# Optimization experiments

Measured on AMD Instinct MI355X. Metric: run time of the kernel, lower is better.

## Reference

```python
import jax, jax.numpy as jnp
import numpy as np
from jax import lax

T, B, C, H, W, NH = 4, 4, 512, 32, 32, 8
HD = C // NH  # head dim 64
EPS = 1e-5
TAU = 2.0

@jax.custom_vjp
def spike(x):
    # Heaviside forward (spikingjelly: x >= 0 -> 1)
    return (x >= 0.0).astype(x.dtype)

def _spike_fwd(x):
    return spike(x), x

def _spike_bwd(x, g):
    # sigmoid surrogate gradient, alpha=4.0 (spikingjelly default)
    s = jax.nn.sigmoid(4.0 * x)
    return (g * 4.0 * s * (1.0 - s),)

spike.defvjp(_spike_fwd, _spike_bwd)

def lif(x, v_th=1.0):
    # MultiStepLIFNode: tau=2, v_reset=0 (hard reset), detach_reset=True.
    # x: [T, ...]; sequential over T via scan.
    def step(v, xt):
        v = v + (xt - v) / TAU
        s = spike(v - v_th)
        v = v * (1.0 - lax.stop_gradient(s))  # detach_reset hard reset
        return v, s
    return lax.scan(step, jnp.zeros_like(x[0]), x)[1]

def bn(x, g, b, m, v):
    # eval-mode BatchNorm1d over channel axis 2 of [T,B,C,N]
    scale = g / jnp.sqrt(v + EPS)
    return (x - m[:, None]) * scale[:, None] + b[:, None]

def setup_inputs() -> dict:
    key = jax.random.key(0)
    ks = jax.random.split(key, 24)
    def w(k):
        return jax.random.normal(k, (C, C), jnp.float32) * (1.0 / np.sqrt(C))
    def bnp(k):
        k1, k2, k3, k4 = jax.random.split(k, 4)
        return (jax.random.normal(k1, (C,), jnp.float32) * 0.1 + 1.0,
                jax.random.normal(k2, (C,), jnp.float32) * 0.1,
                jax.random.normal(k3, (C,), jnp.float32) * 0.1,
                jax.random.uniform(k4, (C,), jnp.float32, 0.5, 1.5))
    q_g, q_b, q_m, q_v = bnp(ks[1])
    k_g, k_b, k_m, k_v = bnp(ks[3])
    v_g, v_b, v_m, v_v = bnp(ks[5])
    p_g, p_b, p_m, p_v = bnp(ks[7])
    return {
        'x': jax.random.normal(ks[0], (T, B, C, H, W), jnp.float32),
        'Wq': w(ks[10]), 'q_g': q_g, 'q_b': q_b, 'q_m': q_m, 'q_v': q_v,
        'Wk': w(ks[11]), 'k_g': k_g, 'k_b': k_b, 'k_m': k_m, 'k_v': k_v,
        'Wv': w(ks[12]), 'v_g': v_g, 'v_b': v_b, 'v_m': v_m, 'v_v': v_v,
        'Wp': w(ks[13]), 'bp': jax.random.normal(ks[14], (C,), jnp.float32) * 0.02,
        'p_g': p_g, 'p_b': p_b, 'p_m': p_m, 'p_v': p_v,
    }

def reference(x, Wq, q_g, q_b, q_m, q_v, Wk, k_g, k_b, k_m, k_v,
              Wv, v_g, v_b, v_m, v_v, Wp, bp, p_g, p_b, p_m, p_v):
    t, b, c, h, w = x.shape
    n = h * w
    xs = lif(x).reshape(t, b, c, n)  # proj_lif -> spikes in {0,1}

    def qkv_branch(Wt, g, bb, m, v):
        y = jnp.einsum('tbcn,dc->tbdn', xs, Wt)  # conv1x1
        y = lif(bn(y, g, bb, m, v))               # bn + lif
        # [T,B,C,N] -> [T,B,heads,N,head_dim]
        return y.reshape(t, b, NH, HD, n).transpose(0, 1, 2, 4, 3)

    q = qkv_branch(Wq, q_g, q_b, q_m, q_v)
    k = qkv_branch(Wk, k_g, k_b, k_m, k_v)
    v = qkv_branch(Wv, v_g, v_b, v_m, v_v)

    attn = jnp.einsum('tbhnd,tbhmd->tbhnm', q, k)           # q @ k^T (binary spikes)
    o = jnp.einsum('tbhnm,tbhmd->tbhnd', attn, v) * 0.125   # attn @ v * 0.125
    o = o.transpose(0, 1, 2, 4, 3).reshape(t, b, c, n)      # [T,B,C,N]
    o = lif(o, v_th=0.5)                                     # attn_lif

    y = jnp.einsum('tbcn,dc->tbdn', o, Wp) + bp[:, None]     # proj conv (bias)
    y = bn(y, p_g, p_b, p_m, p_v)
    return y.reshape(t, b, c, h, w)
```

## Files before the change

kernel.cpp:

```cpp
#include <hip/hip_runtime.h>
#include <hip/hip_bf16.h>
#include <stdint.h>

#define T_  4
#define B_  4
#define C_  512
#define N_  1024
#define NH_ 8
#define HD_ 64
#define NP_ 16384
#define EPS_ 1e-5f

typedef __bf16 bf16_t;
typedef __bf16 bf16x8 __attribute__((ext_vector_type(8)));
typedef float  f32x4  __attribute__((ext_vector_type(4)));
typedef unsigned short u16x4 __attribute__((ext_vector_type(4)));
typedef unsigned char  u8x4  __attribute__((ext_vector_type(4)));
typedef unsigned long long u64;
typedef unsigned int u32;

#define XS_OFF   0ULL
#define AHI_OFF  16777216ULL
#define ALO_OFF  18350080ULL
#define PHI_OFF  19922944ULL
#define PLO_OFF  20447232ULL
#define SC_OFF   20971520ULL
#define SH_OFF   20977664ULL
#define PSC_OFF  20983808ULL
#define PSH_OFF  20985856ULL
#define QS_OFF   20987904ULL
#define KB_OFF   37765120ULL
#define VB_OFF   38813696ULL
#define M2H_OFF  39862272ULL
#define M2L_OFF  40910848ULL

__global__ __launch_bounds__(256) void prep_kernel(
    const float* __restrict__ Wq, const float* __restrict__ Wk,
    const float* __restrict__ Wv, const float* __restrict__ Wp,
    const float* __restrict__ qg, const float* __restrict__ qb, const float* __restrict__ qm, const float* __restrict__ qv,
    const float* __restrict__ kg, const float* __restrict__ kb, const float* __restrict__ km, const float* __restrict__ kv,
    const float* __restrict__ vg, const float* __restrict__ vb, const float* __restrict__ vm, const float* __restrict__ vv,
    const float* __restrict__ bp,
    const float* __restrict__ pg, const float* __restrict__ pb, const float* __restrict__ pm, const float* __restrict__ pv,
    bf16_t* __restrict__ Ahi, bf16_t* __restrict__ Alo,
    bf16_t* __restrict__ Phi, bf16_t* __restrict__ Plo,
    float* __restrict__ scale, float* __restrict__ shift,
    float* __restrict__ pscale, float* __restrict__ pshift)
{
    const int i0 = blockIdx.x * 256 + threadIdx.x;
    const int stride = gridDim.x * 256;
    for (int idx = i0; idx < 1536 * 512; idx += stride) {
        int r = idx >> 9;
        int br = r >> 9;
        const float* W = (br == 0) ? Wq : (br == 1) ? Wk : Wv;
        float w = W[((r & 511) << 9) + (idx & 511)];
        bf16_t h = (bf16_t)w;
        Ahi[idx] = h;
        Alo[idx] = (bf16_t)(w - (float)h);
    }
    for (int idx = i0; idx < 512 * 512; idx += stride) {
        float w = Wp[idx];
        bf16_t h = (bf16_t)w;
        Phi[idx] = h;
        Plo[idx] = (bf16_t)(w - (float)h);
    }
    for (int idx = i0; idx < 1536; idx += stride) {
        int br = idx >> 9, d = idx & 511;
        const float* g  = (br == 0) ? qg : (br == 1) ? kg : vg;
        const float* bb = (br == 0) ? qb : (br == 1) ? kb : vb;
        const float* mm = (br == 0) ? qm : (br == 1) ? km : vm;
        const float* vr = (br == 0) ? qv : (br == 1) ? kv : vv;
        float sc = g[d] / sqrtf(vr[d] + EPS_);
        scale[idx] = sc;
        shift[idx] = bb[d] - mm[d] * sc;
    }
    for (int idx = i0; idx < 512; idx += stride) {
        float sc = pg[idx] / sqrtf(pv[idx] + EPS_);
        pscale[idx] = sc;
        pshift[idx] = (bp[idx] - pm[idx]) * sc + pb[idx];
    }
}

__global__ __launch_bounds__(256) void lif_x_kernel(const float* __restrict__ x,
                                                    bf16_t* __restrict__ xsT)
{
    __shared__ bf16_t St[64 * 72];
    const int tid = threadIdx.x;
    const int nl  = tid & 63;
    const int c4  = tid >> 6;
    const int n0 = blockIdx.x * 64;
    const int c0 = blockIdx.y * 64;
    const int b  = blockIdx.z;
    float v[16];
#pragma unroll
    for (int k = 0; k < 16; ++k) v[k] = 0.f;

    for (int t = 0; t < T_; ++t) {
        bf16x8 s0, s1;
#pragma unroll
        for (int k = 0; k < 16; ++k) {
            float xv = x[(size_t)((t * B_ + b) * C_ + (c0 + c4 * 16 + k)) * N_ + n0 + nl];
            float vn = v[k] + (xv - v[k]) * 0.5f;
            bool s = (vn >= 1.0f);
            v[k] = s ? 0.0f : vn;
            bf16_t sp = s ? (bf16_t)1.0f : (bf16_t)0.0f;
            if (k < 8) s0[k] = sp; else s1[k - 8] = sp;
        }
        __syncthreads();
        *(bf16x8*)&St[nl * 72 + c4 * 16]     = s0;
        *(bf16x8*)&St[nl * 72 + c4 * 16 + 8] = s1;
        __syncthreads();
#pragma unroll
        for (int it = 0; it < 2; ++it) {
            int id = it * 256 + tid;
            int row = id >> 3, sg = id & 7;
            *(bf16x8*)&xsT[((size_t)((t * B_ + b) << 10) + n0 + row) * C_ + c0 + sg * 8] =
                *(const bf16x8*)&St[row * 72 + sg * 8];
        }
    }
}

__global__ __launch_bounds__(256) void gemm_qkv_lif(
    const bf16_t* __restrict__ Ahi, const bf16_t* __restrict__ Alo,
    const bf16_t* __restrict__ xsT,
    const float* __restrict__ scale, const float* __restrict__ shift,
    bf16_t* __restrict__ qsT, u32* __restrict__ kbits, u32* __restrict__ vbits)
{
    __shared__ __align__(16) unsigned char smem[49152];

    const int tid  = threadIdx.x;
    const int lane = tid & 63;
    const int wv   = tid >> 6;
    const int wr   = wv >> 1, wc = wv & 1;
    const int m0   = blockIdx.y * 128;
    const int branch = m0 >> 9;
    const int site0 = blockIdx.x * 32;
    const int b    = site0 >> 10;
    const int n0   = site0 & 1023;

    const int frow = lane & 15;
    const int g4   = lane >> 4;

    f32x4 acc[4][4];
#pragma unroll
    for (int t = 0; t < 4; ++t)
#pragma unroll
        for (int mi = 0; mi < 4; ++mi) acc[t][mi] = f32x4{0.f, 0.f, 0.f, 0.f};

    for (int kk = 0; kk < 512; kk += 64) {
        __syncthreads();
#pragma unroll
        for (int p = 0; p < 4; ++p) {
            int s = p * 256 + tid;
            int row = s >> 3, j = s & 7;
            int kc = (j ^ (row & 7)) << 3;
            size_t goff = (size_t)(m0 + row) * 512 + kk + kc;
            unsigned ldsb = (unsigned)(p * 256 + wv * 64) * 16;
            __builtin_amdgcn_global_load_lds((const __attribute__((address_space(1))) void*)(Ahi + goff),
                                             (__attribute__((address_space(3))) void*)(smem + ldsb), 16, 0, 0);
            __builtin_amdgcn_global_load_lds((const __attribute__((address_space(1))) void*)(Alo + goff),
                                             (__attribute__((address_space(3))) void*)(smem + 16384 + ldsb), 16, 0, 0);
        }
#pragma unroll
        for (int p = 0; p < 4; ++p) {
            int s = p * 256 + tid;
            int t = s >> 8, row = (s >> 3) & 31, j = s & 7;
            int kc = (j ^ (row & 7)) << 3;
            size_t goff = ((size_t)((t * B_ + b) << 10) + n0 + row) * 512 + kk + kc;
            unsigned ldsb = 32768u + (unsigned)(p * 256 + wv * 64) * 16;
            __builtin_amdgcn_global_load_lds((const __attribute__((address_space(1))) void*)(xsT + goff),
                                             (__attribute__((address_space(3))) void*)(smem + ldsb), 16, 0, 0);
        }
        __syncthreads();

#pragma unroll
        for (int ks = 0; ks < 2; ++ks) {
            bf16x8 ah[4], al[4];
#pragma unroll
            for (int mi = 0; mi < 4; ++mi) {
                int row = wr * 64 + mi * 16 + frow;
                int jj = (ks * 4 + g4) ^ (row & 7);
                ah[mi] = *(const bf16x8*)(smem + row * 128 + jj * 16);
                al[mi] = *(const bf16x8*)(smem + 16384 + row * 128 + jj * 16);
            }
#pragma unroll
            for (int t = 0; t < 4; ++t) {
                int rowb = wc * 16 + frow;
                int jj = (ks * 4 + g4) ^ (rowb & 7);
                bf16x8 bb = *(const bf16x8*)(smem + 32768 + t * 4096 + rowb * 128 + jj * 16);
#pragma unroll
                for (int mi = 0; mi < 4; ++mi) {
                    acc[t][mi] = __builtin_amdgcn_mfma_f32_16x16x32_bf16(ah[mi], bb, acc[t][mi], 0, 0, 0);
                    acc[t][mi] = __builtin_amdgcn_mfma_f32_16x16x32_bf16(al[mi], bb, acc[t][mi], 0, 0, 0);
                }
            }
        }
    }

    if (branch == 0) {
        bf16_t* Tt = (bf16_t*)smem;
        u16x4 qpk[4][4];
#pragma unroll
        for (int mi = 0; mi < 4; ++mi)
#pragma unroll
            for (int r = 0; r < 4; ++r) {
                int gr = m0 + wr * 64 + mi * 16 + g4 * 4 + r;
                float sc = scale[gr], sh = shift[gr];
                float vv = 0.f;
#pragma unroll
                for (int t = 0; t < 4; ++t) {
                    float y = acc[t][mi][r] * sc + sh;
                    float vn = vv + (y - vv) * 0.5f;
                    bool s = (vn >= 1.0f);
                    vv = s ? 0.f : vn;
                    qpk[t][mi][r] = s ? 0x3F80 : 0;
                }
            }
#pragma unroll
        for (int t = 0; t < 4; ++t) {
            const int tb = t * B_ + b;
            __syncthreads();
#pragma unroll
            for (int mi = 0; mi < 4; ++mi) {
                int nl = wc * 16 + frow;
                int cl = wr * 64 + mi * 16 + g4 * 4;
                *(u16x4*)&Tt[nl * 136 + cl] = qpk[t][mi];
            }
            __syncthreads();
#pragma unroll
            for (int it = 0; it < 2; ++it) {
                int id = it * 256 + tid;
                int row = id >> 4, sg = id & 15;
                *(bf16x8*)&qsT[((size_t)(tb << 10) + n0 + row) * 512 + m0 + sg * 8] =
                    *(const bf16x8*)&Tt[row * 136 + sg * 8];
            }
        }
    } else {
        unsigned char* Sb = (unsigned char*)smem;
        u32* bdst = (branch == 1) ? kbits : vbits;
        u8x4 kpk[4][4];
#pragma unroll
        for (int mi = 0; mi < 4; ++mi)
#pragma unroll
            for (int r = 0; r < 4; ++r) {
                int gr = m0 + wr * 64 + mi * 16 + g4 * 4 + r;
                float sc = scale[gr], sh = shift[gr];
                float vv = 0.f;
#pragma unroll
                for (int t = 0; t < 4; ++t) {
                    float y = acc[t][mi][r] * sc + sh;
                    float vn = vv + (y - vv) * 0.5f;
                    bool s = (vn >= 1.0f);
                    vv = s ? 0.f : vn;
                    kpk[t][mi][r] = s ? 1 : 0;
                }
            }
#pragma unroll
        for (int t = 0; t < 4; ++t) {
            const int tb = t * B_ + b;
            __syncthreads();
#pragma unroll
            for (int mi = 0; mi < 4; ++mi) {
                int nl = wc * 16 + frow;
                int cl = wr * 64 + mi * 16 + g4 * 4;
                *(u8x4*)&Sb[nl * 132 + cl] = kpk[t][mi];
            }
            __syncthreads();
#pragma unroll
            for (int i = 0; i < 16; ++i) {
                int item = wv * 16 + i;
                int c = item * 2 + (lane >> 5);
                unsigned char vb_ = Sb[(lane & 31) * 132 + c];
                u64 mask = __ballot(vb_ != 0);
                if (lane == 0) {
                    int r0 = (m0 & 511) + item * 2;
                    int r1 = r0 + 1;
                    bdst[((size_t)(tb * NH_ + (r0 >> 6)) * 64 + (r0 & 63)) * 32 + (n0 >> 5)] = (u32)mask;
                    bdst[((size_t)(tb * NH_ + (r1 >> 6)) * 64 + (r1 & 63)) * 32 + (n0 >> 5)] = (u32)(mask >> 32);
                }
            }
        }
    }
}

__global__ __launch_bounds__(256) void gemm_proj(
    const bf16_t* __restrict__ Phi, const bf16_t* __restrict__ Plo,
    const bf16_t* __restrict__ Bm,
    const float* __restrict__ scale, const float* __restrict__ shift,
    float* __restrict__ out)
{
    __shared__ __align__(16) unsigned char smem[49152];

    const int tid  = threadIdx.x;
    const int lane = tid & 63;
    const int wv   = tid >> 6;
    const int wr   = wv >> 1, wc = wv & 1;
    const int m0   = blockIdx.y * 128;
    const int n0   = blockIdx.x * 128;

    const int frow = lane & 15;
    const int g4   = lane >> 4;

    f32x4 acc[4][4];
#pragma unroll
    for (int i = 0; i < 4; ++i)
#pragma unroll
        for (int j = 0; j < 4; ++j) acc[i][j] = f32x4{0.f, 0.f, 0.f, 0.f};

    for (int kk = 0; kk < 512; kk += 64) {
        __syncthreads();
#pragma unroll
        for (int p = 0; p < 4; ++p) {
            int s = p * 256 + tid;
            int row = s >> 3, j = s & 7;
            int kc = (j ^ (row & 7)) << 3;
            size_t goff = (size_t)(m0 + row) * 512 + kk + kc;
            unsigned ldsb = (unsigned)(p * 256 + wv * 64) * 16;
            __builtin_amdgcn_global_load_lds((const __attribute__((address_space(1))) void*)(Phi + goff),
                                             (__attribute__((address_space(3))) void*)(smem + ldsb), 16, 0, 0);
            __builtin_amdgcn_global_load_lds((const __attribute__((address_space(1))) void*)(Plo + goff),
                                             (__attribute__((address_space(3))) void*)(smem + 16384 + ldsb), 16, 0, 0);
        }
#pragma unroll
        for (int p = 0; p < 4; ++p) {
            int s = p * 256 + tid;
            int row = s >> 3, j = s & 7;
            int kc = (j ^ (row & 7)) << 3;
            size_t goff = (size_t)(n0 + row) * 512 + kk + kc;
            unsigned ldsb = 32768u + (unsigned)(p * 256 + wv * 64) * 16;
            __builtin_amdgcn_global_load_lds((const __attribute__((address_space(1))) void*)(Bm + goff),
                                             (__attribute__((address_space(3))) void*)(smem + ldsb), 16, 0, 0);
        }
        __syncthreads();

#pragma unroll
        for (int ks = 0; ks < 2; ++ks) {
            bf16x8 ah[4], al[4];
#pragma unroll
            for (int mi = 0; mi < 4; ++mi) {
                int row = wr * 64 + mi * 16 + frow;
                int jj = (ks * 4 + g4) ^ (row & 7);
                ah[mi] = *(const bf16x8*)(smem + row * 128 + jj * 16);
                al[mi] = *(const bf16x8*)(smem + 16384 + row * 128 + jj * 16);
            }
#pragma unroll
            for (int ni = 0; ni < 4; ++ni) {
                int site = wc * 64 + ni * 16 + frow;
                int jj = (ks * 4 + g4) ^ (site & 7);
                bf16x8 bb = *(const bf16x8*)(smem + 32768 + site * 128 + jj * 16);
#pragma unroll
                for (int mi = 0; mi < 4; ++mi) {
                    acc[mi][ni] = __builtin_amdgcn_mfma_f32_16x16x32_bf16(ah[mi], bb, acc[mi][ni], 0, 0, 0);
                    acc[mi][ni] = __builtin_amdgcn_mfma_f32_16x16x32_bf16(al[mi], bb, acc[mi][ni], 0, 0, 0);
                }
            }
        }
    }

#pragma unroll
    for (int mi = 0; mi < 4; ++mi)
#pragma unroll
        for (int ni = 0; ni < 4; ++ni)
#pragma unroll
            for (int r = 0; r < 4; ++r) {
                int gr = m0 + wr * 64 + mi * 16 + g4 * 4 + r;
                int gc = n0 + wc * 64 + ni * 16 + frow;
                float vout = acc[mi][ni][r] * scale[gr] + shift[gr];
                int tb = gc >> 10, nn = gc & 1023;
                out[((size_t)(tb * C_ + gr)) * N_ + nn] = vout;
            }
}

__global__ __launch_bounds__(256) void m2t_kernel(const u64* __restrict__ kbit,
                                                  const u64* __restrict__ vbit,
                                                  bf16_t* __restrict__ m2h,
                                                  bf16_t* __restrict__ m2l)
{
    __shared__ u64 Kb[64][17];
    __shared__ u64 Vb[64][17];
    __shared__ float M2f[64][64];
    const int tid = threadIdx.x;
    const int h  = blockIdx.x;
    const int tb = blockIdx.y;

    const u64* kbase = kbit + (size_t)(tb * NH_ + h) * 1024;
    const u64* vbase = vbit + (size_t)(tb * NH_ + h) * 1024;
    for (int i = tid; i < 1024; i += 256) {
        Kb[i >> 4][i & 15] = kbase[i];
        Vb[i >> 4][i & 15] = vbase[i];
    }
    __syncthreads();

    const int d1 = tid >> 2, l2 = tid & 3;
    int cnt[16];
#pragma unroll
    for (int jj = 0; jj < 16; ++jj) cnt[jj] = 0;
    for (int w = 0; w < 16; ++w) {
        u64 kw = Kb[d1][w];
#pragma unroll
        for (int jj = 0; jj < 16; ++jj)
            cnt[jj] += __popcll(kw & Vb[l2 + 4 * jj][w]);
    }
#pragma unroll
    for (int jj = 0; jj < 16; ++jj)
        M2f[d1][l2 + 4 * jj] = (float)cnt[jj] * 0.125f;
    __syncthreads();

    const int d2 = tid >> 2, d1b = (tid & 3) * 16;
    bf16x8 h0, h1, l0, l1;
#pragma unroll
    for (int j = 0; j < 16; ++j) {
        float m = M2f[d1b + j][d2];
        bf16_t hi = (bf16_t)m;
        bf16_t lo = (bf16_t)(m - (float)hi);
        if (j < 8) { h0[j] = hi; l0[j] = lo; } else { h1[j - 8] = hi; l1[j - 8] = lo; }
    }
    size_t base = (size_t)(tb * NH_ + h) * 4096 + tid * 16;
    *(bf16x8*)&m2h[base]     = h0;
    *(bf16x8*)&m2h[base + 8] = h1;
    *(bf16x8*)&m2l[base]     = l0;
    *(bf16x8*)&m2l[base + 8] = l1;
}

__global__ __launch_bounds__(256) void o_kernel(const bf16_t* __restrict__ qsT,
                                                const bf16_t* __restrict__ m2h,
                                                const bf16_t* __restrict__ m2l,
                                                bf16_t* __restrict__ osT)
{
    __shared__ bf16_t Ah[64][72];
    __shared__ bf16_t Al[64][72];
    __shared__ bf16_t Bq[128][72];

    const int tid  = threadIdx.x;
    const int lane = tid & 63;
    const int wv   = tid >> 6;
    const int nt = blockIdx.x, h = blockIdx.y, b = blockIdx.z;
    const int n0 = nt * 128;
    const int frow = lane & 15;
    const int g    = lane >> 4;

    float vst[4][2][4];
#pragma unroll
    for (int mi = 0; mi < 4; ++mi)
#pragma unroll
        for (int ni = 0; ni < 2; ++ni)
#pragma unroll
            for (int r = 0; r < 4; ++r) vst[mi][ni][r] = 0.f;

    for (int t = 0; t < T_; ++t) {
        const int tb = t * B_ + b;
        __syncthreads();
        {
            int row = tid >> 2, col = (tid & 3) * 16;
            size_t gbase = (size_t)(tb * NH_ + h) * 4096 + row * 64 + col;
            *(bf16x8*)&Ah[row][col]     = *(const bf16x8*)&m2h[gbase];
            *(bf16x8*)&Ah[row][col + 8] = *(const bf16x8*)&m2h[gbase + 8];
            *(bf16x8*)&Al[row][col]     = *(const bf16x8*)&m2l[gbase];
            *(bf16x8*)&Al[row][col + 8] = *(const bf16x8*)&m2l[gbase + 8];
        }
#pragma unroll
        for (int w = 0; w < 4; ++w) {
            int id = w * 256 + tid;
            int row = id >> 3, cg = (id & 7) * 8;
            *(bf16x8*)&Bq[row][cg] =
                *(const bf16x8*)&qsT[(size_t)((tb << 10) + n0 + row) * C_ + h * 64 + cg];
        }
        __syncthreads();

        bf16x8 afh[4][2], afl[4][2], bfq[2][2];
#pragma unroll
        for (int mi = 0; mi < 4; ++mi)
#pragma unroll
            for (int ks = 0; ks < 2; ++ks) {
                afh[mi][ks] = *(const bf16x8*)&Ah[mi * 16 + frow][ks * 32 + g * 8];
                afl[mi][ks] = *(const bf16x8*)&Al[mi * 16 + frow][ks * 32 + g * 8];
            }
#pragma unroll
        for (int ni = 0; ni < 2; ++ni)
#pragma unroll
            for (int ks = 0; ks < 2; ++ks)
                bfq[ni][ks] = *(const bf16x8*)&Bq[wv * 32 + ni * 16 + frow][ks * 32 + g * 8];

        f32x4 acc[4][2];
#pragma unroll
        for (int mi = 0; mi < 4; ++mi)
#pragma unroll
            for (int ni = 0; ni < 2; ++ni) acc[mi][ni] = f32x4{0.f, 0.f, 0.f, 0.f};

#pragma unroll
        for (int ks = 0; ks < 2; ++ks)
#pragma unroll
            for (int mi = 0; mi < 4; ++mi)
#pragma unroll
                for (int ni = 0; ni < 2; ++ni) {
                    acc[mi][ni] = __builtin_amdgcn_mfma_f32_16x16x32_bf16(afh[mi][ks], bfq[ni][ks], acc[mi][ni], 0, 0, 0);
                    acc[mi][ni] = __builtin_amdgcn_mfma_f32_16x16x32_bf16(afl[mi][ks], bfq[ni][ks], acc[mi][ni], 0, 0, 0);
                }

#pragma unroll
        for (int mi = 0; mi < 4; ++mi)
#pragma unroll
            for (int ni = 0; ni < 2; ++ni) {
                ushort4 pk;
                unsigned short* pp = &pk.x;
#pragma unroll
                for (int r = 0; r < 4; ++r) {
                    float o = acc[mi][ni][r];
                    float vn = vst[mi][ni][r] + (o - vst[mi][ni][r]) * 0.5f;
                    bool s = (vn >= 0.5f);
                    vst[mi][ni][r] = s ? 0.f : vn;
                    pp[r] = s ? 0x3F80 : 0;
                }
                size_t off = (size_t)((tb << 10) + n0 + wv * 32 + ni * 16 + frow) * C_
                           + h * 64 + mi * 16 + g * 4;
                *(ushort4*)&osT[off] = pk;
            }
    }
}

extern "C" void kernel_launch(void* const* d_in, const int* in_sizes, int n_in,
                              void* d_out, int out_size, void* d_ws, size_t ws_size,
                              hipStream_t stream)
{
    const float* x   = (const float*)d_in[0];
    const float* Wq  = (const float*)d_in[1];
    const float* qg  = (const float*)d_in[2];
    const float* qb  = (const float*)d_in[3];
    const float* qm  = (const float*)d_in[4];
    const float* qv  = (const float*)d_in[5];
    const float* Wk  = (const float*)d_in[6];
    const float* kg  = (const float*)d_in[7];
    const float* kb  = (const float*)d_in[8];
    const float* km  = (const float*)d_in[9];
    const float* kv  = (const float*)d_in[10];
    const float* Wv  = (const float*)d_in[11];
    const float* vg  = (const float*)d_in[12];
    const float* vb  = (const float*)d_in[13];
    const float* vm  = (const float*)d_in[14];
    const float* vv  = (const float*)d_in[15];
    const float* Wp  = (const float*)d_in[16];
    const float* bp  = (const float*)d_in[17];
    const float* pg  = (const float*)d_in[18];
    const float* pb  = (const float*)d_in[19];
    const float* pm  = (const float*)d_in[20];
    const float* pv  = (const float*)d_in[21];

    char* ws = (char*)d_ws;
    bf16_t* xsT    = (bf16_t*)(ws + XS_OFF);
    bf16_t* Ahi    = (bf16_t*)(ws + AHI_OFF);
    bf16_t* Alo    = (bf16_t*)(ws + ALO_OFF);
    bf16_t* Phi    = (bf16_t*)(ws + PHI_OFF);
    bf16_t* Plo    = (bf16_t*)(ws + PLO_OFF);
    float*  scv    = (float*)(ws + SC_OFF);
    float*  shv    = (float*)(ws + SH_OFF);
    float*  psc    = (float*)(ws + PSC_OFF);
    float*  psh    = (float*)(ws + PSH_OFF);
    bf16_t* qsT    = (bf16_t*)(ws + QS_OFF);
    u32*    kbits32= (u32*)(ws + KB_OFF);
    u32*    vbits32= (u32*)(ws + VB_OFF);
    u64*    kbits  = (u64*)(ws + KB_OFF);
    u64*    vbits  = (u64*)(ws + VB_OFF);
    bf16_t* m2h    = (bf16_t*)(ws + M2H_OFF);
    bf16_t* m2l    = (bf16_t*)(ws + M2L_OFF);
    bf16_t* osT    = (bf16_t*)(ws + XS_OFF);
    float*  out    = (float*)d_out;

    prep_kernel<<<dim3(3072), dim3(256), 0, stream>>>(
        Wq, Wk, Wv, Wp, qg, qb, qm, qv, kg, kb, km, kv, vg, vb, vm, vv,
        bp, pg, pb, pm, pv, Ahi, Alo, Phi, Plo, scv, shv, psc, psh);

    lif_x_kernel<<<dim3(16, 8, 4), dim3(256), 0, stream>>>(x, xsT);

    gemm_qkv_lif<<<dim3(128, 12), dim3(256), 0, stream>>>(
        Ahi, Alo, xsT, scv, shv, qsT, kbits32, vbits32);

    m2t_kernel<<<dim3(8, 16), dim3(256), 0, stream>>>(kbits, vbits, m2h, m2l);

    o_kernel<<<dim3(8, 8, 4), dim3(256), 0, stream>>>(qsT, m2h, m2l, osT);

    gemm_proj<<<dim3(128, 4), dim3(256), 0, stream>>>(Phi, Plo, osT, psc, psh, out);

    (void)in_sizes; (void)n_in; (void)out_size; (void)ws_size;
}
```

Baseline: 216.6 us.

## Fuse weight prep into LIF kernel and stage o_kernel output through LDS

Weight and BN-parameter preparation now runs as an extra z-slice of blocks inside the x-LIF kernel, which removes one kernel launch and lets the prep work overlap with the LIF work. The o_kernel tile shrinks from 128 to 64 tokens per block, doubling the grid. Its spike outputs are written to shared memory and then stored as coalesced 16-byte rows instead of scattered 8-byte stores. In exchange, each block does less work per load of the m2 matrices and pays an extra barrier per timestep.

Result: no change. 213.8 us (-1.3%).

```diff
diff --git a/kernel.cpp b/kernel.cpp
--- a/kernel.cpp
+++ b/kernel.cpp
@@ -34,7 +34,8 @@
 #define M2H_OFF  39862272ULL
 #define M2L_OFF  40910848ULL
 
-__global__ __launch_bounds__(256) void prep_kernel(
+__global__ __launch_bounds__(256) void prep_lif_kernel(
+    const float* __restrict__ x, bf16_t* __restrict__ xsT,
     const float* __restrict__ Wq, const float* __restrict__ Wk,
     const float* __restrict__ Wv, const float* __restrict__ Wp,
     const float* __restrict__ qg, const float* __restrict__ qb, const float* __restrict__ qm, const float* __restrict__ qv,
@@ -47,45 +48,45 @@
     float* __restrict__ scale, float* __restrict__ shift,
     float* __restrict__ pscale, float* __restrict__ pshift)
 {
-    const int i0 = blockIdx.x * 256 + threadIdx.x;
-    const int stride = gridDim.x * 256;
-    for (int idx = i0; idx < 1536 * 512; idx += stride) {
-        int r = idx >> 9;
-        int br = r >> 9;
-        const float* W = (br == 0) ? Wq : (br == 1) ? Wk : Wv;
-        float w = W[((r & 511) << 9) + (idx & 511)];
-        bf16_t h = (bf16_t)w;
-        Ahi[idx] = h;
-        Alo[idx] = (bf16_t)(w - (float)h);
-    }
-    for (int idx = i0; idx < 512 * 512; idx += stride) {
-        float w = Wp[idx];
-        bf16_t h = (bf16_t)w;
-        Phi[idx] = h;
-        Plo[idx] = (bf16_t)(w - (float)h);
-    }
-    for (int idx = i0; idx < 1536; idx += stride) {
-        int br = idx >> 9, d = idx & 511;
-        const float* g  = (br == 0) ? qg : (br == 1) ? kg : vg;
-        const float* bb = (br == 0) ? qb : (br == 1) ? kb : vb;
-        const float* mm = (br == 0) ? qm : (br == 1) ? km : vm;
-        const float* vr = (br == 0) ? qv : (br == 1) ? kv : vv;
-        float sc = g[d] / sqrtf(vr[d] + EPS_);
-        scale[idx] = sc;
-        shift[idx] = bb[d] - mm[d] * sc;
-    }
-    for (int idx = i0; idx < 512; idx += stride) {
-        float sc = pg[idx] / sqrtf(pv[idx] + EPS_);
-        pscale[idx] = sc;
-        pshift[idx] = (bp[idx] - pm[idx]) * sc + pb[idx];
-    }
-}
-
-__global__ __launch_bounds__(256) void lif_x_kernel(const float* __restrict__ x,
-                                                    bf16_t* __restrict__ xsT)
-{
     __shared__ bf16_t St[64 * 72];
     const int tid = threadIdx.x;
+
+    if (blockIdx.z == 4) {
+        const int i0 = (blockIdx.y * 16 + blockIdx.x) * 256 + tid;
+        const int stride = 128 * 256;
+        for (int idx = i0; idx < 1536 * 512; idx += stride) {
+            int r = idx >> 9;
+            int br = r >> 9;
+            const float* W = (br == 0) ? Wq : (br == 1) ? Wk : Wv;
+            float w = W[((r & 511) << 9) + (idx & 511)];
+            bf16_t h = (bf16_t)w;
+            Ahi[idx] = h;
+            Alo[idx] = (bf16_t)(w - (float)h);
+        }
+        for (int idx = i0; idx < 512 * 512; idx += stride) {
+            float w = Wp[idx];
+            bf16_t h = (bf16_t)w;
+            Phi[idx] = h;
+            Plo[idx] = (bf16_t)(w - (float)h);
+        }
+        for (int idx = i0; idx < 1536; idx += stride) {
+            int br = idx >> 9, d = idx & 511;
+            const float* g  = (br == 0) ? qg : (br == 1) ? kg : vg;
+            const float* bb = (br == 0) ? qb : (br == 1) ? kb : vb;
+            const float* mm = (br == 0) ? qm : (br == 1) ? km : vm;
+            const float* vr = (br == 0) ? qv : (br == 1) ? kv : vv;
+            float sc = g[d] / sqrtf(vr[d] + EPS_);
+            scale[idx] = sc;
+            shift[idx] = bb[d] - mm[d] * sc;
+        }
+        for (int idx = i0; idx < 512; idx += stride) {
+            float sc = pg[idx] / sqrtf(pv[idx] + EPS_);
+            pscale[idx] = sc;
+            pshift[idx] = (bp[idx] - pm[idx]) * sc + pb[idx];
+        }
+        return;
+    }
+
     const int nl  = tid & 63;
     const int c4  = tid >> 6;
     const int n0 = blockIdx.x * 64;
@@ -429,23 +430,22 @@
 {
     __shared__ bf16_t Ah[64][72];
     __shared__ bf16_t Al[64][72];
-    __shared__ bf16_t Bq[128][72];
+    __shared__ bf16_t Bq[64][72];
+    __shared__ bf16_t Ot[64][72];
 
     const int tid  = threadIdx.x;
     const int lane = tid & 63;
     const int wv   = tid >> 6;
     const int nt = blockIdx.x, h = blockIdx.y, b = blockIdx.z;
-    const int n0 = nt * 128;
+    const int n0 = nt * 64;
     const int frow = lane & 15;
     const int g    = lane >> 4;
 
-    float vst[4][2][4];
+    float vst[4][4];
 #pragma unroll
     for (int mi = 0; mi < 4; ++mi)
 #pragma unroll
-        for (int ni = 0; ni < 2; ++ni)
-#pragma unroll
-            for (int r = 0; r < 4; ++r) vst[mi][ni][r] = 0.f;
+        for (int r = 0; r < 4; ++r) vst[mi][r] = 0.f;
 
     for (int t = 0; t < T_; ++t) {
         const int tb = t * B_ + b;
@@ -459,15 +459,15 @@
             *(bf16x8*)&Al[row][col + 8] = *(const bf16x8*)&m2l[gbase + 8];
         }
 #pragma unroll
-        for (int w = 0; w < 4; ++w) {
-            int id = w * 256 + tid;
+        for (int it = 0; it < 2; ++it) {
+            int id = it * 256 + tid;
             int row = id >> 3, cg = (id & 7) * 8;
             *(bf16x8*)&Bq[row][cg] =
                 *(const bf16x8*)&qsT[(size_t)((tb << 10) + n0 + row) * C_ + h * 64 + cg];
         }
         __syncthreads();
 
-        bf16x8 afh[4][2], afl[4][2], bfq[2][2];
+        bf16x8 afh[4][2], afl[4][2], bfq[2];
 #pragma unroll
         for (int mi = 0; mi < 4; ++mi)
 #pragma unroll
@@ -476,45 +476,43 @@
                 afl[mi][ks] = *(const bf16x8*)&Al[mi * 16 + frow][ks * 32 + g * 8];
             }
 #pragma unroll
-        for (int ni = 0; ni < 2; ++ni)
-#pragma unroll
-            for (int ks = 0; ks < 2; ++ks)
-                bfq[ni][ks] = *(const bf16x8*)&Bq[wv * 32 + ni * 16 + frow][ks * 32 + g * 8];
-
-        f32x4 acc[4][2];
-#pragma unroll
-        for (int mi = 0; mi < 4; ++mi)
-#pragma unroll
-            for (int ni = 0; ni < 2; ++ni) acc[mi][ni] = f32x4{0.f, 0.f, 0.f, 0.f};
-
-#pragma unroll
         for (int ks = 0; ks < 2; ++ks)
-#pragma unroll
-            for (int mi = 0; mi < 4; ++mi)
-#pragma unroll
-                for (int ni = 0; ni < 2; ++ni) {
-                    acc[mi][ni] = __builtin_amdgcn_mfma_f32_16x16x32_bf16(afh[mi][ks], bfq[ni][ks], acc[mi][ni], 0, 0, 0);
-                    acc[mi][ni] = __builtin_amdgcn_mfma_f32_16x16x32_bf16(afl[mi][ks], bfq[ni][ks], acc[mi][ni], 0, 0, 0);
-                }
-
-#pragma unroll
-        for (int mi = 0; mi < 4; ++mi)
-#pragma unroll
-            for (int ni = 0; ni < 2; ++ni) {
-                ushort4 pk;
-                unsigned short* pp = &pk.x;
-#pragma unroll
-                for (int r = 0; r < 4; ++r) {
-                    float o = acc[mi][ni][r];
-                    float vn = vst[mi][ni][r] + (o - vst[mi][ni][r]) * 0.5f;
-                    bool s = (vn >= 0.5f);
-                    vst[mi][ni][r] = s ? 0.f : vn;
-                    pp[r] = s ? 0x3F80 : 0;
-                }
-                size_t off = (size_t)((tb << 10) + n0 + wv * 32 + ni * 16 + frow) * C_
-                           + h * 64 + mi * 16 + g * 4;
-                *(ushort4*)&osT[off] = pk;
-            }
+            bfq[ks] = *(const bf16x8*)&Bq[wv * 16 + frow][ks * 32 + g * 8];
+
+        f32x4 acc[4];
+#pragma unroll
+        for (int mi = 0; mi < 4; ++mi) acc[mi] = f32x4{0.f, 0.f, 0.f, 0.f};
+
+#pragma unroll
+        for (int ks = 0; ks < 2; ++ks)
+#pragma unroll
+            for (int mi = 0; mi < 4; ++mi) {
+                acc[mi] = __builtin_amdgcn_mfma_f32_16x16x32_bf16(afh[mi][ks], bfq[ks], acc[mi], 0, 0, 0);
+                acc[mi] = __builtin_amdgcn_mfma_f32_16x16x32_bf16(afl[mi][ks], bfq[ks], acc[mi], 0, 0, 0);
+            }
+
+#pragma unroll
+        for (int mi = 0; mi < 4; ++mi) {
+            u16x4 pk;
+#pragma unroll
+            for (int r = 0; r < 4; ++r) {
+                float o = acc[mi][r];
+                float vn = vst[mi][r] + (o - vst[mi][r]) * 0.5f;
+                bool s = (vn >= 0.5f);
+                vst[mi][r] = s ? 0.f : vn;
+                pk[r] = s ? 0x3F80 : 0;
+            }
+            *(u16x4*)&Ot[wv * 16 + frow][mi * 16 + g * 4] = pk;
+        }
+        __syncthreads();
+
+#pragma unroll
+        for (int it = 0; it < 2; ++it) {
+            int id = it * 256 + tid;
+            int row = id >> 3, sg = (id & 7) * 8;
+            *(bf16x8*)&osT[(size_t)((tb << 10) + n0 + row) * C_ + h * 64 + sg] =
+                *(const bf16x8*)&Ot[row][sg];
+        }
     }
 }
 
@@ -565,18 +563,16 @@
     bf16_t* osT    = (bf16_t*)(ws + XS_OFF);
     float*  out    = (float*)d_out;
 
-    prep_kernel<<<dim3(3072), dim3(256), 0, stream>>>(
-        Wq, Wk, Wv, Wp, qg, qb, qm, qv, kg, kb, km, kv, vg, vb, vm, vv,
+    prep_lif_kernel<<<dim3(16, 8, 5), dim3(256), 0, stream>>>(
+        x, xsT, Wq, Wk, Wv, Wp, qg, qb, qm, qv, kg, kb, km, kv, vg, vb, vm, vv,
         bp, pg, pb, pm, pv, Ahi, Alo, Phi, Plo, scv, shv, psc, psh);
-
-    lif_x_kernel<<<dim3(16, 8, 4), dim3(256), 0, stream>>>(x, xsT);
 
     gemm_qkv_lif<<<dim3(128, 12), dim3(256), 0, stream>>>(
         Ahi, Alo, xsT, scv, shv, qsT, kbits32, vbits32);
 
     m2t_kernel<<<dim3(8, 16), dim3(256), 0, stream>>>(kbits, vbits, m2h, m2l);
 
-    o_kernel<<<dim3(8, 8, 4), dim3(256), 0, stream>>>(qsT, m2h, m2l, osT);
+    o_kernel<<<dim3(16, 8, 4), dim3(256), 0, stream>>>(qsT, m2h, m2l, osT);
 
     gemm_proj<<<dim3(128, 4), dim3(256), 0, stream>>>(Phi, Plo, osT, psc, psh, out);
 
```
